# Optimization experiments

Hardware: AMD Instinct MI355X
Metric: run time of the kernel (lower is better)

Reference implementation:

```python
import jax, jax.numpy as jnp
import numpy as np

B, S, D, H = 128, 1024, 512, 512


def setup_inputs() -> dict:
    key = jax.random.key(0)
    ks = jax.random.split(key, 8)
    return {
        "input": jax.random.normal(ks[0], (B, D), jnp.float32),
        "context": jax.random.normal(ks[1], (B, S, D), jnp.float32),
        "mask": jax.random.randint(ks[2], (B, S), 0, 2).astype(bool),
        "W_in": jax.random.normal(ks[3], (H, D), jnp.float32) * (1.0 / np.sqrt(D)),
        "b_in": jax.random.normal(ks[4], (H,), jnp.float32) * 0.01,
        "W_ctx": jax.random.normal(ks[5], (H, D), jnp.float32) * (1.0 / np.sqrt(D)),
        "b_ctx": jax.random.normal(ks[6], (H,), jnp.float32) * 0.01,
        "V": jax.random.uniform(ks[7], (H,), jnp.float32, -1.0, 1.0),
    }


def reference(input, context, mask, W_in, b_in, W_ctx, b_ctx, V):
    # inp: [B, H] -> broadcast over S (torch: unsqueeze(2).expand)
    inp = input @ W_in.T + b_in
    # 1x1 Conv1d over permuted context == per-position linear: [B, H, S]
    ctx = jnp.einsum('bsd,hd->bhs', context, W_ctx) + b_ctx[None, :, None]
    # additive (Bahdanau) score: V . tanh(inp + ctx) over H -> [B, S]
    att = jnp.einsum('h,bhs->bs', V, jnp.tanh(inp[:, :, None] + ctx))
    att = jnp.where(mask, -jnp.inf, att)
    alpha = jax.nn.softmax(att, axis=-1)  # [B, S]
    # weighted sum of projected context: [B, H]
    hidden_state = jnp.einsum('bhs,bs->bh', ctx, alpha)
    return (hidden_state, alpha)
```

## Files before the change

kernel.cpp:

```cpp
#include <hip/hip_runtime.h>
#include <math.h>

#define B_ 128
#define S_ 1024
#define D_ 512
#define H_ 512

typedef _Float16 f16x4 __attribute__((ext_vector_type(4)));
typedef _Float16 f16x8 __attribute__((ext_vector_type(8)));
typedef float    f32x4 __attribute__((ext_vector_type(4)));

#if defined(__has_builtin)
#if __has_builtin(__builtin_amdgcn_global_load_lds)
#define HAVE_GLDS 1
#endif
#endif
#ifndef HAVE_GLDS
#define HAVE_GLDS 0
#endif

__global__ void zero_k(float* __restrict__ p, int n) {
    int i = blockIdx.x * 256 + threadIdx.x;
    if (i < n) p[i] = 0.f;
}

__global__ __launch_bounds__(256) void cvt16_k(const float* __restrict__ src,
                                               _Float16* __restrict__ dst, int n8) {
    int i = blockIdx.x * 256 + threadIdx.x;
    if (i < n8) {
        float4 a = ((const float4*)src)[2 * i];
        float4 b = ((const float4*)src)[2 * i + 1];
        f16x8 r;
        r[0] = (_Float16)a.x; r[1] = (_Float16)a.y;
        r[2] = (_Float16)a.z; r[3] = (_Float16)a.w;
        r[4] = (_Float16)b.x; r[5] = (_Float16)b.y;
        r[6] = (_Float16)b.z; r[7] = (_Float16)b.w;
        *(f16x8*)(dst + (size_t)8 * i) = r;
    }
}

__global__ __launch_bounds__(256) void linear_k(const float* __restrict__ X,
                                                const float* __restrict__ W,
                                                const float* __restrict__ bias,
                                                float* __restrict__ out) {
    int idx = blockIdx.x * 256 + threadIdx.x;
    int b = idx >> 9;
    int h = idx & 511;
    const float4* x = (const float4*)(X + (size_t)b * D_);
    const float4* w = (const float4*)(W + (size_t)h * D_);
    float s = 0.f;
#pragma unroll 8
    for (int k = 0; k < D_ / 4; ++k) {
        float4 xv = x[k], wv = w[k];
        s = fmaf(xv.x, wv.x, s);
        s = fmaf(xv.y, wv.y, s);
        s = fmaf(xv.z, wv.z, s);
        s = fmaf(xv.w, wv.w, s);
    }
    out[idx] = s + bias[h];
}

__device__ inline f16x8 cvt8(float4 a, float4 b) {
    f16x8 r;
    r[0] = (_Float16)a.x; r[1] = (_Float16)a.y;
    r[2] = (_Float16)a.z; r[3] = (_Float16)a.w;
    r[4] = (_Float16)b.x; r[5] = (_Float16)b.y;
    r[6] = (_Float16)b.z; r[7] = (_Float16)b.w;
    return r;
}

__device__ inline float fast_tanh(float x) {
    float e = __expf(2.f * x);
    return 1.f - 2.f / (e + 1.f);
}

__device__ inline void stage16(const _Float16* g, _Float16* l, int lane) {
#if HAVE_GLDS
    __builtin_amdgcn_global_load_lds((__attribute__((address_space(1))) void*)g,
                                     (__attribute__((address_space(3))) void*)l,
                                     16, 0, 0);
#else
    f16x8 v = *(const f16x8*)g;
    *(f16x8*)((char*)l + lane * 16) = v;
#endif
}

__global__ __launch_bounds__(256) void score16(const _Float16* __restrict__ ctx16,
                                               const _Float16* __restrict__ Wc16,
                                               const float* __restrict__ bc,
                                               const float* __restrict__ Vv,
                                               const float* __restrict__ inp,
                                               float* __restrict__ att) {
    __shared__ __align__(16) _Float16 Ah[2][128][32];
    __shared__ __align__(16) _Float16 Bh[2][128][32];
    __shared__ float red[8][128];

    const int tid = threadIdx.x;
    const int s0 = blockIdx.x * 128;
    const int h0 = blockIdx.y * 128;
    const int b  = blockIdx.z;

    const int wave = tid >> 6;
    const int lane = tid & 63;
    const int wm = wave >> 1, wn = wave & 1;
    const int l15 = lane & 15, quad = lane >> 4;

    const int rrow = lane >> 2;
    const int rgr  = lane & 3;
    const _Float16* Ag = Wc16 + (size_t)(h0 + wave * 32 + rrow) * D_ + rgr * 8;
    const _Float16* Bg = ctx16 + ((size_t)b * S_ + s0 + wave * 32 + rrow) * D_ + rgr * 8;

    f32x4 acc[4][4];
#pragma unroll
    for (int mi = 0; mi < 4; ++mi)
#pragma unroll
        for (int ni = 0; ni < 4; ++ni) acc[mi][ni] = (f32x4){0.f, 0.f, 0.f, 0.f};

#define STAGE(bf, k0) do {                                                      \
    stage16(Ag + (k0),            &Ah[bf][wave * 32][0],      lane);            \
    stage16(Ag + (k0) + 16 * D_,  &Ah[bf][wave * 32 + 16][0], lane);            \
    stage16(Bg + (k0),            &Bh[bf][wave * 32][0],      lane);            \
    stage16(Bg + (k0) + 16 * D_,  &Bh[bf][wave * 32 + 16][0], lane); } while (0)

#define COMPUTE(bf) do {                                                        \
    f16x8 bhf_[4];                                                              \
    _Pragma("unroll")                                                           \
    for (int ni = 0; ni < 4; ++ni)                                              \
        bhf_[ni] = *(const f16x8*)&Bh[bf][wn * 64 + ni * 16 + l15][quad * 8];   \
    _Pragma("unroll")                                                           \
    for (int mi = 0; mi < 4; ++mi) {                                            \
        f16x8 ah_ = *(const f16x8*)&Ah[bf][wm * 64 + mi * 16 + l15][quad * 8];  \
        _Pragma("unroll")                                                       \
        for (int ni = 0; ni < 4; ++ni)                                          \
            acc[mi][ni] = __builtin_amdgcn_mfma_f32_16x16x32_f16(ah_, bhf_[ni], \
                                                                 acc[mi][ni], 0, 0, 0); \
    } } while (0)

    STAGE(0, 0);
    __syncthreads();
#pragma unroll
    for (int it = 0; it < 16; ++it) {
        if (it + 1 < 16) STAGE((it + 1) & 1, (it + 1) * 32);
        COMPUTE(it & 1);
        __syncthreads();
    }
#undef STAGE
#undef COMPUTE

    float p[4] = {0.f, 0.f, 0.f, 0.f};
#pragma unroll
    for (int mi = 0; mi < 4; ++mi) {
#pragma unroll
        for (int r = 0; r < 4; ++r) {
            const int h = h0 + wm * 64 + mi * 16 + quad * 4 + r;
            const float c  = inp[(size_t)b * H_ + h] + bc[h];
            const float vh = Vv[h];
#pragma unroll
            for (int ni = 0; ni < 4; ++ni)
                p[ni] = fmaf(vh, fast_tanh(c + acc[mi][ni][r]), p[ni]);
        }
    }
    const int cid = wm * 4 + quad;
#pragma unroll
    for (int ni = 0; ni < 4; ++ni)
        red[cid][wn * 64 + ni * 16 + l15] = p[ni];
    __syncthreads();
    if (tid < 128) {
        float s = 0.f;
#pragma unroll
        for (int g = 0; g < 8; ++g) s += red[g][tid];
        atomicAdd(att + (size_t)b * S_ + s0 + tid, s);
    }
}

__global__ __launch_bounds__(256) void score_f32(const float* __restrict__ ctx,
                                                 const float* __restrict__ Wc,
                                                 const float* __restrict__ bc,
                                                 const float* __restrict__ Vv,
                                                 const float* __restrict__ inp,
                                                 float* __restrict__ att) {
    __shared__ __align__(16) _Float16 Ah[2][128][32];
    __shared__ __align__(16) _Float16 Bh[2][128][32];
    __shared__ float red[8][128];

    const int tid = threadIdx.x;
    const int s0 = blockIdx.x * 128;
    const int h0 = blockIdx.y * 128;
    const int b  = blockIdx.z;

    const int r0  = tid >> 2;
    const int kg  = tid & 3;
    const int swz = ((kg ^ (r0 & 3)) << 3);

    const int wave = tid >> 6;
    const int lane = tid & 63;
    const int wm = wave >> 1, wn = wave & 1;
    const int l15 = lane & 15, quad = lane >> 4;
    const int rdsw = ((quad ^ (l15 & 3)) << 3);

    const float* Arow0 = Wc  + (size_t)(h0 + r0) * D_ + kg * 8;
    const float* Arow1 = Arow0 + (size_t)64 * D_;
    const float* Brow0 = ctx + ((size_t)b * S_ + s0 + r0) * D_ + kg * 8;
    const float* Brow1 = Brow0 + (size_t)64 * D_;

    f32x4 acc[4][4];
#pragma unroll
    for (int mi = 0; mi < 4; ++mi)
#pragma unroll
        for (int ni = 0; ni < 4; ++ni) acc[mi][ni] = (f32x4){0.f, 0.f, 0.f, 0.f};

    float4 A0a, A0b, A1a, A1b, B0a, B0b, B1a, B1b;

#define LOADS(step) do { const int kk_ = (step) * 32;                               \
    A0a = *(const float4*)(Arow0 + kk_); A0b = *(const float4*)(Arow0 + kk_ + 4);   \
    A1a = *(const float4*)(Arow1 + kk_); A1b = *(const float4*)(Arow1 + kk_ + 4);   \
    B0a = *(const float4*)(Brow0 + kk_); B0b = *(const float4*)(Brow0 + kk_ + 4);   \
    B1a = *(const float4*)(Brow1 + kk_); B1b = *(const float4*)(Brow1 + kk_ + 4); } while (0)

#define WRITE(bf) do {                                                              \
    *(f16x8*)&Ah[bf][r0][swz]      = cvt8(A0a, A0b);                                \
    *(f16x8*)&Ah[bf][r0 + 64][swz] = cvt8(A1a, A1b);                                \
    *(f16x8*)&Bh[bf][r0][swz]      = cvt8(B0a, B0b);                                \
    *(f16x8*)&Bh[bf][r0 + 64][swz] = cvt8(B1a, B1b); } while (0)

#define COMPUTE(bf) do {                                                            \
    f16x8 bhf_[4];                                                                  \
    _Pragma("unroll")                                                               \
    for (int ni = 0; ni < 4; ++ni)                                                  \
        bhf_[ni] = *(const f16x8*)&Bh[bf][wn * 64 + ni * 16 + l15][rdsw];           \
    _Pragma("unroll")                                                               \
    for (int mi = 0; mi < 4; ++mi) {                                                \
        f16x8 ah_ = *(const f16x8*)&Ah[bf][wm * 64 + mi * 16 + l15][rdsw];          \
        _Pragma("unroll")                                                           \
        for (int ni = 0; ni < 4; ++ni)                                              \
            acc[mi][ni] = __builtin_amdgcn_mfma_f32_16x16x32_f16(ah_, bhf_[ni],     \
                                                                 acc[mi][ni], 0, 0, 0); \
    } } while (0)

    LOADS(0);
    WRITE(0);
    LOADS(1);
    __syncthreads();

    for (int it = 0; it < 16; it += 2) {
        COMPUTE(0);
        WRITE(1);
        if (it + 2 < 16) LOADS(it + 2);
        __syncthreads();
        COMPUTE(1);
        if (it + 2 < 16) WRITE(0);
        if (it + 3 < 16) LOADS(it + 3);
        __syncthreads();
    }
#undef LOADS
#undef WRITE
#undef COMPUTE

    float p[4] = {0.f, 0.f, 0.f, 0.f};
#pragma unroll
    for (int mi = 0; mi < 4; ++mi) {
#pragma unroll
        for (int r = 0; r < 4; ++r) {
            const int h = h0 + wm * 64 + mi * 16 + quad * 4 + r;
            const float c  = inp[(size_t)b * H_ + h] + bc[h];
            const float vh = Vv[h];
#pragma unroll
            for (int ni = 0; ni < 4; ++ni)
                p[ni] = fmaf(vh, fast_tanh(c + acc[mi][ni][r]), p[ni]);
        }
    }
    const int cid = wm * 4 + quad;
#pragma unroll
    for (int ni = 0; ni < 4; ++ni)
        red[cid][wn * 64 + ni * 16 + l15] = p[ni];
    __syncthreads();
    if (tid < 128) {
        float s = 0.f;
#pragma unroll
        for (int g = 0; g < 8; ++g) s += red[g][tid];
        atomicAdd(att + (size_t)b * S_ + s0 + tid, s);
    }
}

__global__ __launch_bounds__(256) void softmax_k(const float* __restrict__ att,
                                                 const int* __restrict__ mask,
                                                 float* __restrict__ alpha) {
    const int b = blockIdx.x;
    const int t = threadIdx.x;
    __shared__ float sm[256];
    float v[4];
    float mx = -INFINITY;
#pragma unroll
    for (int i = 0; i < 4; ++i) {
        int s = t + i * 256;
        float a = att[(size_t)b * S_ + s];
        int mk = mask[(size_t)b * S_ + s];
        v[i] = mk ? -INFINITY : a;
        mx = fmaxf(mx, v[i]);
    }
    sm[t] = mx;
    __syncthreads();
    for (int off = 128; off > 0; off >>= 1) {
        if (t < off) sm[t] = fmaxf(sm[t], sm[t + off]);
        __syncthreads();
    }
    mx = sm[0];
    __syncthreads();
    float e[4];
    float sum = 0.f;
#pragma unroll
    for (int i = 0; i < 4; ++i) {
        e[i] = expf(v[i] - mx);
        sum += e[i];
    }
    sm[t] = sum;
    __syncthreads();
    for (int off = 128; off > 0; off >>= 1) {
        if (t < off) sm[t] += sm[t + off];
        __syncthreads();
    }
    float inv = 1.f / sm[0];
#pragma unroll
    for (int i = 0; i < 4; ++i) alpha[(size_t)b * S_ + t + i * 256] = e[i] * inv;
}

__global__ __launch_bounds__(256) void cbarh_k(const _Float16* __restrict__ src16,
                                               const float* __restrict__ alpha,
                                               float* __restrict__ out) {
    const int b  = blockIdx.y;
    const int s0 = blockIdx.x * 128;
    const int t  = threadIdx.x;
    const int w = t >> 6, lane = t & 63;
    __shared__ float al[128];
    __shared__ float red[3][512];
    if (t < 128) al[t] = alpha[(size_t)b * S_ + s0 + t];
    __syncthreads();
    const _Float16* base = src16 + ((size_t)b * S_ + s0) * D_ + lane * 8;
    float acc[8] = {0.f, 0.f, 0.f, 0.f, 0.f, 0.f, 0.f, 0.f};
#pragma unroll 4
    for (int s = w; s < 128; s += 4) {
        float a = al[s];
        f16x8 v = *(const f16x8*)(base + (size_t)s * D_);
#pragma unroll
        for (int j = 0; j < 8; ++j) acc[j] = fmaf(a, (float)v[j], acc[j]);
    }
    if (w > 0) {
#pragma unroll
        for (int j = 0; j < 8; ++j) red[w - 1][lane * 8 + j] = acc[j];
    }
    __syncthreads();
    if (w == 0) {
        float* dst = out + (size_t)b * D_ + lane * 8;
#pragma unroll
        for (int j = 0; j < 8; ++j)
            atomicAdd(dst + j, acc[j] + red[0][lane * 8 + j] + red[1][lane * 8 + j] + red[2][lane * 8 + j]);
    }
}

__global__ __launch_bounds__(256) void cbar_k(const float* __restrict__ ctx,
                                              const float* __restrict__ alpha,
                                              float* __restrict__ cbar) {
    const int b = blockIdx.y;
    const int s0 = blockIdx.x * 128;
    const int t = threadIdx.x;
    const int c4 = t & 127;
    const int sh = t >> 7;
    __shared__ float al[128];
    __shared__ float4 red[128];
    if (t < 128) al[t] = alpha[(size_t)b * S_ + s0 + t];
    __syncthreads();
    const float4* base = (const float4*)(ctx + ((size_t)b * S_ + s0) * D_);
    float4 c = {0.f, 0.f, 0.f, 0.f};
#pragma unroll 4
    for (int s = sh; s < 128; s += 2) {
        float a = al[s];
        float4 x = base[(size_t)s * (D_ / 4) + c4];
        c.x = fmaf(a, x.x, c.x);
        c.y = fmaf(a, x.y, c.y);
        c.z = fmaf(a, x.z, c.z);
        c.w = fmaf(a, x.w, c.w);
    }
    if (sh == 1) red[c4] = c;
    __syncthreads();
    if (sh == 0) {
        float4 o = red[c4];
        float* dst = cbar + (size_t)b * D_ + c4 * 4;
        atomicAdd(dst + 0, c.x + o.x);
        atomicAdd(dst + 1, c.y + o.y);
        atomicAdd(dst + 2, c.z + o.z);
        atomicAdd(dst + 3, c.w + o.w);
    }
}

extern "C" void kernel_launch(void* const* d_in, const int* in_sizes, int n_in,
                              void* d_out, int out_size, void* d_ws, size_t ws_size,
                              hipStream_t stream) {
    const float* input = (const float*)d_in[0];
    const float* ctx   = (const float*)d_in[1];
    const int*   mask  = (const int*)d_in[2];
    const float* W_in  = (const float*)d_in[3];
    const float* b_in  = (const float*)d_in[4];
    const float* W_ctx = (const float*)d_in[5];
    const float* b_ctx = (const float*)d_in[6];
    const float* V     = (const float*)d_in[7];

    float* hidden = (float*)d_out;
    float* alpha  = (float*)d_out + B_ * H_;

    float* inp  = (float*)d_ws;
    float* att  = inp + B_ * H_;
    float* cbar = att + B_ * S_;
    _Float16* ctx16 = (_Float16*)(cbar + B_ * D_);
    _Float16* Wc16  = ctx16 + (size_t)B_ * S_ * D_;

    const size_t base_bytes = (size_t)(B_ * H_ + B_ * S_ + B_ * D_) * sizeof(float);
    const size_t f16_bytes  = ((size_t)B_ * S_ * D_ + (size_t)H_ * D_) * sizeof(_Float16);
    const bool big = ws_size >= base_bytes + f16_bytes;

    dim3 g2(S_ / 128, H_ / 128, B_);
    dim3 g4(S_ / 128, B_);
    const int nz = B_ * S_ + B_ * D_;

    if (big) {
        zero_k<<<(nz + 255) / 256, 256, 0, stream>>>(att, nz);

        cvt16_k<<<(B_ * S_ * D_ / 8 + 255) / 256, 256, 0, stream>>>(ctx, ctx16, B_ * S_ * D_ / 8);
        cvt16_k<<<(H_ * D_ / 8 + 255) / 256, 256, 0, stream>>>(W_ctx, Wc16, H_ * D_ / 8);

        linear_k<<<(B_ * H_) / 256, 256, 0, stream>>>(input, W_in, b_in, inp);

        score16<<<g2, 256, 0, stream>>>(ctx16, Wc16, b_ctx, V, inp, att);

        softmax_k<<<B_, 256, 0, stream>>>(att, mask, alpha);

        cbarh_k<<<g4, 256, 0, stream>>>(ctx16, alpha, cbar);

        linear_k<<<(B_ * H_) / 256, 256, 0, stream>>>(cbar, W_ctx, b_ctx, hidden);
    } else {
        zero_k<<<(nz + 255) / 256, 256, 0, stream>>>(att, nz);

        linear_k<<<(B_ * H_) / 256, 256, 0, stream>>>(input, W_in, b_in, inp);

        score_f32<<<g2, 256, 0, stream>>>(ctx, W_ctx, b_ctx, V, inp, att);

        softmax_k<<<B_, 256, 0, stream>>>(att, mask, alpha);

        cbar_k<<<g4, 256, 0, stream>>>(ctx, alpha, cbar);

        linear_k<<<(B_ * H_) / 256, 256, 0, stream>>>(cbar, W_ctx, b_ctx, hidden);
    }
}
```

Before: 570.2 us.

## Load MFMA fragments directly from global memory and split linear dot products across lanes

```diff
diff --git a/kernel.cpp b/kernel.cpp
--- a/kernel.cpp
+++ b/kernel.cpp
@@ -9,15 +9,6 @@
 typedef _Float16 f16x4 __attribute__((ext_vector_type(4)));
 typedef _Float16 f16x8 __attribute__((ext_vector_type(8)));
 typedef float    f32x4 __attribute__((ext_vector_type(4)));
-
-#if defined(__has_builtin)
-#if __has_builtin(__builtin_amdgcn_global_load_lds)
-#define HAVE_GLDS 1
-#endif
-#endif
-#ifndef HAVE_GLDS
-#define HAVE_GLDS 0
-#endif
 
 __global__ void zero_k(float* __restrict__ p, int n) {
     int i = blockIdx.x * 256 + threadIdx.x;
@@ -39,25 +30,28 @@
     }
 }
 
-__global__ __launch_bounds__(256) void linear_k(const float* __restrict__ X,
-                                                const float* __restrict__ W,
-                                                const float* __restrict__ bias,
-                                                float* __restrict__ out) {
-    int idx = blockIdx.x * 256 + threadIdx.x;
-    int b = idx >> 9;
-    int h = idx & 511;
+__global__ __launch_bounds__(256) void linear4_k(const float* __restrict__ X,
+                                                 const float* __restrict__ W,
+                                                 const float* __restrict__ bias,
+                                                 float* __restrict__ out) {
+    int g   = blockIdx.x * 64 + (threadIdx.x >> 2);
+    int sub = threadIdx.x & 3;
+    int b = g >> 9;
+    int h = g & 511;
     const float4* x = (const float4*)(X + (size_t)b * D_);
     const float4* w = (const float4*)(W + (size_t)h * D_);
     float s = 0.f;
 #pragma unroll 8
-    for (int k = 0; k < D_ / 4; ++k) {
+    for (int k = sub; k < D_ / 4; k += 4) {
         float4 xv = x[k], wv = w[k];
         s = fmaf(xv.x, wv.x, s);
         s = fmaf(xv.y, wv.y, s);
         s = fmaf(xv.z, wv.z, s);
         s = fmaf(xv.w, wv.w, s);
     }
-    out[idx] = s + bias[h];
+    s += __shfl_xor(s, 1);
+    s += __shfl_xor(s, 2);
+    if (sub == 0) out[g] = s + bias[h];
 }
 
 __device__ inline f16x8 cvt8(float4 a, float4 b) {
@@ -74,25 +68,12 @@
     return 1.f - 2.f / (e + 1.f);
 }
 
-__device__ inline void stage16(const _Float16* g, _Float16* l, int lane) {
-#if HAVE_GLDS
-    __builtin_amdgcn_global_load_lds((__attribute__((address_space(1))) void*)g,
-                                     (__attribute__((address_space(3))) void*)l,
-                                     16, 0, 0);
-#else
-    f16x8 v = *(const f16x8*)g;
-    *(f16x8*)((char*)l + lane * 16) = v;
-#endif
-}
-
 __global__ __launch_bounds__(256) void score16(const _Float16* __restrict__ ctx16,
                                                const _Float16* __restrict__ Wc16,
                                                const float* __restrict__ bc,
                                                const float* __restrict__ Vv,
                                                const float* __restrict__ inp,
                                                float* __restrict__ att) {
-    __shared__ __align__(16) _Float16 Ah[2][128][32];
-    __shared__ __align__(16) _Float16 Bh[2][128][32];
     __shared__ float red[8][128];
 
     const int tid = threadIdx.x;
@@ -105,10 +86,14 @@
     const int wm = wave >> 1, wn = wave & 1;
     const int l15 = lane & 15, quad = lane >> 4;
 
-    const int rrow = lane >> 2;
-    const int rgr  = lane & 3;
-    const _Float16* Ag = Wc16 + (size_t)(h0 + wave * 32 + rrow) * D_ + rgr * 8;
-    const _Float16* Bg = ctx16 + ((size_t)b * S_ + s0 + wave * 32 + rrow) * D_ + rgr * 8;
+    const _Float16* Ab[4];
+    const _Float16* Bb[4];
+#pragma unroll
+    for (int mi = 0; mi < 4; ++mi)
+        Ab[mi] = Wc16 + (size_t)(h0 + wm * 64 + mi * 16 + l15) * D_ + quad * 8;
+#pragma unroll
+    for (int ni = 0; ni < 4; ++ni)
+        Bb[ni] = ctx16 + ((size_t)b * S_ + s0 + wn * 64 + ni * 16 + l15) * D_ + quad * 8;
 
     f32x4 acc[4][4];
 #pragma unroll
@@ -116,36 +101,43 @@
 #pragma unroll
         for (int ni = 0; ni < 4; ++ni) acc[mi][ni] = (f32x4){0.f, 0.f, 0.f, 0.f};
 
-#define STAGE(bf, k0) do {                                                      \
-    stage16(Ag + (k0),            &Ah[bf][wave * 32][0],      lane);            \
-    stage16(Ag + (k0) + 16 * D_,  &Ah[bf][wave * 32 + 16][0], lane);            \
-    stage16(Bg + (k0),            &Bh[bf][wave * 32][0],      lane);            \
-    stage16(Bg + (k0) + 16 * D_,  &Bh[bf][wave * 32 + 16][0], lane); } while (0)
-
-#define COMPUTE(bf) do {                                                        \
-    f16x8 bhf_[4];                                                              \
-    _Pragma("unroll")                                                           \
-    for (int ni = 0; ni < 4; ++ni)                                              \
-        bhf_[ni] = *(const f16x8*)&Bh[bf][wn * 64 + ni * 16 + l15][quad * 8];   \
-    _Pragma("unroll")                                                           \
-    for (int mi = 0; mi < 4; ++mi) {                                            \
-        f16x8 ah_ = *(const f16x8*)&Ah[bf][wm * 64 + mi * 16 + l15][quad * 8];  \
-        _Pragma("unroll")                                                       \
-        for (int ni = 0; ni < 4; ++ni)                                          \
-            acc[mi][ni] = __builtin_amdgcn_mfma_f32_16x16x32_f16(ah_, bhf_[ni], \
-                                                                 acc[mi][ni], 0, 0, 0); \
-    } } while (0)
-
-    STAGE(0, 0);
-    __syncthreads();
-#pragma unroll
-    for (int it = 0; it < 16; ++it) {
-        if (it + 1 < 16) STAGE((it + 1) & 1, (it + 1) * 32);
-        COMPUTE(it & 1);
-        __syncthreads();
-    }
-#undef STAGE
-#undef COMPUTE
+    f16x8 afA[4], bfA[4], afB[4], bfB[4];
+#pragma unroll
+    for (int i = 0; i < 4; ++i) {
+        afA[i] = *(const f16x8*)(Ab[i]);
+        bfA[i] = *(const f16x8*)(Bb[i]);
+    }
+
+#pragma unroll
+    for (int k = 0; k < 16; ++k) {
+        if (k & 1) {
+            if (k + 1 < 16) {
+#pragma unroll
+                for (int i = 0; i < 4; ++i) {
+                    afA[i] = *(const f16x8*)(Ab[i] + (k + 1) * 32);
+                    bfA[i] = *(const f16x8*)(Bb[i] + (k + 1) * 32);
+                }
+            }
+#pragma unroll
+            for (int mi = 0; mi < 4; ++mi)
+#pragma unroll
+                for (int ni = 0; ni < 4; ++ni)
+                    acc[mi][ni] = __builtin_amdgcn_mfma_f32_16x16x32_f16(afB[mi], bfB[ni],
+                                                                         acc[mi][ni], 0, 0, 0);
+        } else {
+#pragma unroll
+            for (int i = 0; i < 4; ++i) {
+                afB[i] = *(const f16x8*)(Ab[i] + (k + 1) * 32);
+                bfB[i] = *(const f16x8*)(Bb[i] + (k + 1) * 32);
+            }
+#pragma unroll
+            for (int mi = 0; mi < 4; ++mi)
+#pragma unroll
+                for (int ni = 0; ni < 4; ++ni)
+                    acc[mi][ni] = __builtin_amdgcn_mfma_f32_16x16x32_f16(afA[mi], bfA[ni],
+                                                                         acc[mi][ni], 0, 0, 0);
+        }
+    }
 
     float p[4] = {0.f, 0.f, 0.f, 0.f};
 #pragma unroll
@@ -427,7 +419,7 @@
         cvt16_k<<<(B_ * S_ * D_ / 8 + 255) / 256, 256, 0, stream>>>(ctx, ctx16, B_ * S_ * D_ / 8);
         cvt16_k<<<(H_ * D_ / 8 + 255) / 256, 256, 0, stream>>>(W_ctx, Wc16, H_ * D_ / 8);
 
-        linear_k<<<(B_ * H_) / 256, 256, 0, stream>>>(input, W_in, b_in, inp);
+        linear4_k<<<(B_ * H_) / 64, 256, 0, stream>>>(input, W_in, b_in, inp);
 
         score16<<<g2, 256, 0, stream>>>(ctx16, Wc16, b_ctx, V, inp, att);
 
@@ -435,11 +427,11 @@
 
         cbarh_k<<<g4, 256, 0, stream>>>(ctx16, alpha, cbar);
 
-        linear_k<<<(B_ * H_) / 256, 256, 0, stream>>>(cbar, W_ctx, b_ctx, hidden);
+        linear4_k<<<(B_ * H_) / 64, 256, 0, stream>>>(cbar, W_ctx, b_ctx, hidden);
     } else {
         zero_k<<<(nz + 255) / 256, 256, 0, stream>>>(att, nz);
 
-        linear_k<<<(B_ * H_) / 256, 256, 0, stream>>>(input, W_in, b_in, inp);
+        linear4_k<<<(B_ * H_) / 64, 256, 0, stream>>>(input, W_in, b_in, inp);
 
         score_f32<<<g2, 256, 0, stream>>>(ctx, W_ctx, b_ctx, V, inp, att);
 
@@ -447,6 +439,6 @@
 
         cbar_k<<<g4, 256, 0, stream>>>(ctx, alpha, cbar);
 
-        linear_k<<<(B_ * H_) / 256, 256, 0, stream>>>(cbar, W_ctx, b_ctx, hidden);
-    }
-}
+        linear4_k<<<(B_ * H_) / 64, 256, 0, stream>>>(cbar, W_ctx, b_ctx, hidden);
+    }
+}
```

Result: slower. 681.1 us (+19.4%).
